# Performance work log

Hardware: AMD Instinct MI355X
Metric: run time of the kernel (lower is better)

Reference implementation:

```python
import itertools
import jax, jax.numpy as jnp
import numpy as np

GRID = 16384      # self.shape = (GRID,)
LAYERS = 8        # num_layers
SPAN = 2          # span = (2,)
K = 2 * SPAN + 1  # kernel size = 5 (ninputs)
NPOS = 2 ** K     # 32 possible boolean input combos
BATCH = 32
M = 4096          # x width; GRID % M == 0
STRIDE = GRID // M

# bitmask: all 2^K boolean input combinations, shape (NPOS, K)
_BITMASK = jnp.asarray(list(itertools.product(range(2), repeat=K)), dtype=jnp.float32)


def setup_inputs() -> dict:
    key = jax.random.key(0)
    k1, k2 = jax.random.split(key)
    x = jax.random.uniform(k1, (BATCH, M), dtype=jnp.float32)
    toggle_gates = jax.random.uniform(k2, (LAYERS, NPOS, GRID), dtype=jnp.float32)
    return {"x": x, "toggle_gates": toggle_gates}


def _convolve(state):
    # torch convolve(): offsets 0..K-1 via wrap-around roll, then spatial roll by
    # -SPAN to center the window -> neighbor n+i-SPAN (mod GRID) at kernel idx i.
    # jnp.roll(state, SPAN - i) gives out[:, n] = state[:, n + i - SPAN mod GRID].
    return jnp.stack([jnp.roll(state, SPAN - i, axis=1) for i in range(K)], axis=-1)  # (B, N, K)


def reference(x, toggle_gates):
    tw = jax.nn.sigmoid(toggle_gates)  # (L, NPOS, N)
    # embed(): scatter x evenly into the grid, rest is scratch (zeros)
    state = jnp.zeros((x.shape[0], GRID), dtype=x.dtype).at[:, ::STRIDE].set(x)

    def step(s, tw_layer):
        conv = _convolve(s)  # (B, N, K)
        # weight[c, b, n] = prod_i (1 - |bitmask[c, i] - conv[b, n, i]|)
        w = jnp.prod(1.0 - jnp.abs(_BITMASK[:, None, None, :] - conv[None]), axis=-1)  # (C, B, N)
        new = jnp.clip(jnp.einsum('cbn,cn->bn', w, tw_layer), 0.0, 1.0)
        return new, None

    state, _ = jax.lax.scan(step, state, tw)
    # forward returns state[slices] = state[:, ::STRIDE]
    return state[:, ::STRIDE]
```

## Files before the change

### kernel.cpp

```cpp
#include <hip/hip_runtime.h>

#define GRID_N 16384
#define NLAYERS 8
#define NPOS 32
#define BATCH 32
#define MW 4096
#define TILE 32
#define HALO 16
#define WBUF 64
#define TWPAD 33

__global__ __launch_bounds__(256) void ASIC_44186623541335_kernel(
    const float* __restrict__ x,
    const float* __restrict__ tg,
    float* __restrict__ out)
{
    __shared__ float st[BATCH][WBUF];
    __shared__ float twl[WBUF][TWPAD];

    const int tid = threadIdx.x;
    const int tx  = tid & 63;
    const int ty  = tid >> 6;
    const int start = blockIdx.x * TILE;
    const int gcol  = (start - HALO + tx) & (GRID_N - 1);

    float pf[8];

    #pragma unroll
    for (int k = 0; k < 8; ++k) {
        const int c = ty + 4 * k;
        pf[k] = tg[(size_t)c * GRID_N + gcol];
    }

    for (int f = tid; f < BATCH * WBUF; f += 256) {
        const int b = f >> 6;
        const int j = f & 63;
        const int g = (start - HALO + j) & (GRID_N - 1);
        st[b][j] = ((g & 3) == 0) ? x[b * MW + (g >> 2)] : 0.0f;
    }

    #pragma unroll
    for (int k = 0; k < 8; ++k) {
        const int c = ty + 4 * k;
        twl[tx][c] = __builtin_amdgcn_rcpf(1.0f + __expf(-pf[k]));
    }
    #pragma unroll
    for (int k = 0; k < 8; ++k) {
        const int c = ty + 4 * k;
        pf[k] = tg[(size_t)NPOS * GRID_N + (size_t)c * GRID_N + gcol];
    }
    __syncthreads();

    float newv[8];
    for (int l = 0; l < NLAYERS; ++l) {
        const int h     = 2 * (NLAYERS - 1 - l);
        const int ncols = TILE + 2 * h;
        const int j     = (HALO - h) + tx;
        const bool act  = tx < ncols;

        if (act) {
            float tw[32];
            #pragma unroll
            for (int c = 0; c < 32; ++c) tw[c] = twl[j][c];

            #pragma unroll
            for (int bb = 0; bb < 8; ++bb) {
                const int b = ty * 8 + bb;
                const float s0 = st[b][j - 2];
                const float s1 = st[b][j - 1];
                const float s2 = st[b][j];
                const float s3 = st[b][j + 1];
                const float s4 = st[b][j + 2];

                float u[16];
                #pragma unroll
                for (int r = 0; r < 16; ++r)
                    u[r] = fmaf(s0, tw[16 + r] - tw[r], tw[r]);
                #pragma unroll
                for (int r = 0; r < 8; ++r)
                    u[r] = fmaf(s1, u[8 + r] - u[r], u[r]);
                #pragma unroll
                for (int r = 0; r < 4; ++r)
                    u[r] = fmaf(s2, u[4 + r] - u[r], u[r]);
                #pragma unroll
                for (int r = 0; r < 2; ++r)
                    u[r] = fmaf(s3, u[2 + r] - u[r], u[r]);
                float res = fmaf(s4, u[1] - u[0], u[0]);
                newv[bb] = fminf(fmaxf(res, 0.0f), 1.0f);
            }
        }
        __syncthreads();

        if (act) {
            #pragma unroll
            for (int bb = 0; bb < 8; ++bb)
                st[ty * 8 + bb][j] = newv[bb];
        }
        if (l < NLAYERS - 1) {
            #pragma unroll
            for (int k = 0; k < 8; ++k) {
                const int c = ty + 4 * k;
                twl[tx][c] = __builtin_amdgcn_rcpf(1.0f + __expf(-pf[k]));
            }
            if (l + 2 < NLAYERS) {
                const float* tn = tg + (size_t)(l + 2) * NPOS * GRID_N;
                #pragma unroll
                for (int k = 0; k < 8; ++k) {
                    const int c = ty + 4 * k;
                    pf[k] = tn[(size_t)c * GRID_N + gcol];
                }
            }
        }
        __syncthreads();
    }

    if (tx < TILE && (tx & 3) == 0) {
        const int m = (start + tx) >> 2;
        #pragma unroll
        for (int bb = 0; bb < 8; ++bb) {
            const int b = ty * 8 + bb;
            out[b * MW + m] = st[b][HALO + tx];
        }
    }
}

extern "C" void kernel_launch(void* const* d_in, const int* in_sizes, int n_in,
                              void* d_out, int out_size, void* d_ws, size_t ws_size,
                              hipStream_t stream) {
    const float* x  = (const float*)d_in[0];
    const float* tg = (const float*)d_in[1];
    float* out = (float*)d_out;
    ASIC_44186623541335_kernel<<<GRID_N / TILE, 256, 0, stream>>>(x, tg, out);
}
```

Before: 81.79 us.

## Double-buffer state and gates in transposed layout with 512 threads and float4 LDS

Doubles the block to 512 threads, so each thread handles 4 batch rows instead of 8. The state is stored transposed ([col][batch]) and both state and sigmoid-gate tiles are double-buffered, which removes one of the two barriers per layer. Loads and stores use float4 LDS accesses, and the gate differences are hoisted out of the batch loop. This aims to raise parallelism and cut LDS instruction count and barrier cost, at the price of more shared memory and register pressure under launch_bounds(512,4).

```diff
diff --git a/kernel.cpp b/kernel.cpp
--- a/kernel.cpp
+++ b/kernel.cpp
@@ -8,119 +8,139 @@
 #define TILE 32
 #define HALO 16
 #define WBUF 64
-#define TWPAD 33
+#define ROWP 36
 
-__global__ __launch_bounds__(256) void ASIC_44186623541335_kernel(
+struct F2 { float a, b; };
+
+__global__ __launch_bounds__(512, 4) void ASIC_44186623541335_kernel(
     const float* __restrict__ x,
     const float* __restrict__ tg,
     float* __restrict__ out)
 {
-    __shared__ float st[BATCH][WBUF];
-    __shared__ float twl[WBUF][TWPAD];
+    __shared__ __align__(16) float st[2][WBUF][ROWP];
+    __shared__ __align__(16) float twl[2][WBUF][ROWP];
 
     const int tid = threadIdx.x;
     const int tx  = tid & 63;
     const int ty  = tid >> 6;
+    const int c0  = 4 * ty;
     const int start = blockIdx.x * TILE;
     const int gcol  = (start - HALO + tx) & (GRID_N - 1);
 
-    float pf[8];
+    float pf[4];
+    #pragma unroll
+    for (int k = 0; k < 4; ++k)
+        pf[k] = tg[(size_t)(c0 + k) * GRID_N + gcol];
 
-    #pragma unroll
-    for (int k = 0; k < 8; ++k) {
-        const int c = ty + 4 * k;
-        pf[k] = tg[(size_t)c * GRID_N + gcol];
+    for (int f = tid; f < WBUF * BATCH; f += 512) {
+        const int j = f >> 5;
+        const int b = f & 31;
+        const int g = (start - HALO + j) & (GRID_N - 1);
+        st[0][j][b] = ((g & 3) == 0) ? x[b * MW + (g >> 2)] : 0.0f;
     }
 
-    for (int f = tid; f < BATCH * WBUF; f += 256) {
-        const int b = f >> 6;
-        const int j = f & 63;
-        const int g = (start - HALO + j) & (GRID_N - 1);
-        st[b][j] = ((g & 3) == 0) ? x[b * MW + (g >> 2)] : 0.0f;
-    }
-
-    #pragma unroll
-    for (int k = 0; k < 8; ++k) {
-        const int c = ty + 4 * k;
-        twl[tx][c] = __builtin_amdgcn_rcpf(1.0f + __expf(-pf[k]));
-    }
-    #pragma unroll
-    for (int k = 0; k < 8; ++k) {
-        const int c = ty + 4 * k;
-        pf[k] = tg[(size_t)NPOS * GRID_N + (size_t)c * GRID_N + gcol];
+    {
+        float4 sg;
+        sg.x = __builtin_amdgcn_rcpf(1.0f + __expf(-pf[0]));
+        sg.y = __builtin_amdgcn_rcpf(1.0f + __expf(-pf[1]));
+        sg.z = __builtin_amdgcn_rcpf(1.0f + __expf(-pf[2]));
+        sg.w = __builtin_amdgcn_rcpf(1.0f + __expf(-pf[3]));
+        *(float4*)&twl[0][tx][c0] = sg;
+        #pragma unroll
+        for (int k = 0; k < 4; ++k)
+            pf[k] = tg[(size_t)NPOS * GRID_N + (size_t)(c0 + k) * GRID_N + gcol];
     }
     __syncthreads();
 
-    float newv[8];
+    #pragma unroll
     for (int l = 0; l < NLAYERS; ++l) {
         const int h     = 2 * (NLAYERS - 1 - l);
         const int ncols = TILE + 2 * h;
         const int j     = (HALO - h) + tx;
-        const bool act  = tx < ncols;
+        const int rb    = l & 1, wb = rb ^ 1;
 
-        if (act) {
+        if (l < NLAYERS - 1) {
+            float4 sg;
+            sg.x = __builtin_amdgcn_rcpf(1.0f + __expf(-pf[0]));
+            sg.y = __builtin_amdgcn_rcpf(1.0f + __expf(-pf[1]));
+            sg.z = __builtin_amdgcn_rcpf(1.0f + __expf(-pf[2]));
+            sg.w = __builtin_amdgcn_rcpf(1.0f + __expf(-pf[3]));
+            *(float4*)&twl[wb][tx][c0] = sg;
+        }
+        if (l + 2 < NLAYERS) {
+            const float* tn = tg + (size_t)(l + 2) * NPOS * GRID_N;
+            #pragma unroll
+            for (int k = 0; k < 4; ++k)
+                pf[k] = tn[(size_t)(c0 + k) * GRID_N + gcol];
+        }
+
+        if (tx < ncols) {
             float tw[32];
             #pragma unroll
-            for (int c = 0; c < 32; ++c) tw[c] = twl[j][c];
+            for (int k = 0; k < 8; ++k) {
+                const float4 q = *(const float4*)&twl[rb][j][4 * k];
+                tw[4 * k]     = q.x; tw[4 * k + 1] = q.y;
+                tw[4 * k + 2] = q.z; tw[4 * k + 3] = q.w;
+            }
+            float d0[16];
+            #pragma unroll
+            for (int r = 0; r < 16; ++r) d0[r] = tw[16 + r] - tw[r];
 
+            float4 S0 = *(const float4*)&st[rb][j - 2][c0];
+            float4 S1 = *(const float4*)&st[rb][j - 1][c0];
+            float4 S2 = *(const float4*)&st[rb][j    ][c0];
+            float4 S3 = *(const float4*)&st[rb][j + 1][c0];
+            float4 S4 = *(const float4*)&st[rb][j + 2][c0];
+
+            float4 res;
             #pragma unroll
-            for (int bb = 0; bb < 8; ++bb) {
-                const int b = ty * 8 + bb;
-                const float s0 = st[b][j - 2];
-                const float s1 = st[b][j - 1];
-                const float s2 = st[b][j];
-                const float s3 = st[b][j + 1];
-                const float s4 = st[b][j + 2];
+            for (int p = 0; p < 2; ++p) {
+                const float s0a = p ? S0.z : S0.x, s0b = p ? S0.w : S0.y;
+                const float s1a = p ? S1.z : S1.x, s1b = p ? S1.w : S1.y;
+                const float s2a = p ? S2.z : S2.x, s2b = p ? S2.w : S2.y;
+                const float s3a = p ? S3.z : S3.x, s3b = p ? S3.w : S3.y;
+                const float s4a = p ? S4.z : S4.x, s4b = p ? S4.w : S4.y;
 
-                float u[16];
+                F2 u[16];
                 #pragma unroll
-                for (int r = 0; r < 16; ++r)
-                    u[r] = fmaf(s0, tw[16 + r] - tw[r], tw[r]);
+                for (int r = 0; r < 16; ++r) {
+                    u[r].a = fmaf(s0a, d0[r], tw[r]);
+                    u[r].b = fmaf(s0b, d0[r], tw[r]);
+                }
                 #pragma unroll
-                for (int r = 0; r < 8; ++r)
-                    u[r] = fmaf(s1, u[8 + r] - u[r], u[r]);
+                for (int r = 0; r < 8; ++r) {
+                    const float da = u[8 + r].a - u[r].a, db = u[8 + r].b - u[r].b;
+                    u[r].a = fmaf(s1a, da, u[r].a);
+                    u[r].b = fmaf(s1b, db, u[r].b);
+                }
                 #pragma unroll
-                for (int r = 0; r < 4; ++r)
-                    u[r] = fmaf(s2, u[4 + r] - u[r], u[r]);
+                for (int r = 0; r < 4; ++r) {
+                    const float da = u[4 + r].a - u[r].a, db = u[4 + r].b - u[r].b;
+                    u[r].a = fmaf(s2a, da, u[r].a);
+                    u[r].b = fmaf(s2b, db, u[r].b);
+                }
                 #pragma unroll
-                for (int r = 0; r < 2; ++r)
-                    u[r] = fmaf(s3, u[2 + r] - u[r], u[r]);
-                float res = fmaf(s4, u[1] - u[0], u[0]);
-                newv[bb] = fminf(fmaxf(res, 0.0f), 1.0f);
+                for (int r = 0; r < 2; ++r) {
+                    const float da = u[2 + r].a - u[r].a, db = u[2 + r].b - u[r].b;
+                    u[r].a = fmaf(s3a, da, u[r].a);
+                    u[r].b = fmaf(s3b, db, u[r].b);
+                }
+                const float da = u[1].a - u[0].a, db = u[1].b - u[0].b;
+                float ra = fmaf(s4a, da, u[0].a);
+                float rbv = fmaf(s4b, db, u[0].b);
+                ra  = fminf(fmaxf(ra, 0.0f), 1.0f);
+                rbv = fminf(fmaxf(rbv, 0.0f), 1.0f);
+                if (p) { res.z = ra; res.w = rbv; } else { res.x = ra; res.y = rbv; }
             }
-        }
-        __syncthreads();
-
-        if (act) {
-            #pragma unroll
-            for (int bb = 0; bb < 8; ++bb)
-                st[ty * 8 + bb][j] = newv[bb];
-        }
-        if (l < NLAYERS - 1) {
-            #pragma unroll
-            for (int k = 0; k < 8; ++k) {
-                const int c = ty + 4 * k;
-                twl[tx][c] = __builtin_amdgcn_rcpf(1.0f + __expf(-pf[k]));
-            }
-            if (l + 2 < NLAYERS) {
-                const float* tn = tg + (size_t)(l + 2) * NPOS * GRID_N;
-                #pragma unroll
-                for (int k = 0; k < 8; ++k) {
-                    const int c = ty + 4 * k;
-                    pf[k] = tn[(size_t)c * GRID_N + gcol];
-                }
-            }
+            *(float4*)&st[wb][j][c0] = res;
         }
         __syncthreads();
     }
 
-    if (tx < TILE && (tx & 3) == 0) {
-        const int m = (start + tx) >> 2;
-        #pragma unroll
-        for (int bb = 0; bb < 8; ++bb) {
-            const int b = ty * 8 + bb;
-            out[b * MW + m] = st[b][HALO + tx];
-        }
+    if (tid < 256) {
+        const int c4 = tid & 7;
+        const int b  = tid >> 3;
+        out[b * MW + (start >> 2) + c4] = st[0][HALO + 4 * c4][b];
     }
 }
 
@@ -130,5 +150,5 @@
     const float* x  = (const float*)d_in[0];
     const float* tg = (const float*)d_in[1];
     float* out = (float*)d_out;
-    ASIC_44186623541335_kernel<<<GRID_N / TILE, 256, 0, stream>>>(x, tg, out);
+    ASIC_44186623541335_kernel<<<GRID_N / TILE, 512, 0, stream>>>(x, tg, out);
 }
```

After: 81.24 us. About the same (-0.7%).
